# Optimization experiments

Measured on AMD Instinct MI355X. Metric: run time of the kernel, lower is better.

The kernel has to match this reference:

```python
import jax, jax.numpy as jnp
import numpy as np

G, N, E, I, H, O = 128, 1024, 64, 128, 128, 128
EPS = 1e-5


def setup_inputs() -> dict:
    key = jax.random.key(0)
    ks = jax.random.split(key, 6)
    return {
        "feature": jax.random.normal(ks[0], (G, N, I), dtype=jnp.float32),
        "eigen": jax.random.normal(ks[1], (G, N, E), dtype=jnp.float32),
        "weights1": jax.random.normal(ks[2], (E, I, H), dtype=jnp.float32),
        "biases1": jnp.zeros((E, H), dtype=jnp.float32),
        "weights2": jax.random.normal(ks[3], (E, H, O), dtype=jnp.float32),
        "biases2": jnp.zeros((E, O), dtype=jnp.float32),
        "bn_gamma": jnp.ones((O,), dtype=jnp.float32),
        "bn_beta": jnp.zeros((O,), dtype=jnp.float32),
    }


def reference(feature, eigen, weights1, biases1, weights2, biases2, bn_gamma, bn_beta):
    # Eigen projection per graph: [G,E,I]
    spec_in = jnp.einsum('gni,gne->gei', feature, eigen)
    # Per-eigen MLP (grouped small GEMMs)
    spec_hidden = jax.nn.relu(jnp.einsum('eik,gei->gek', weights1, spec_in) + biases1)
    spec_out = jnp.einsum('eko,gek->geo', weights2, spec_hidden) + biases2
    # Inverse projection back to nodes: [G,N,O]
    h = jnp.einsum('geo,gne->gno', spec_out, eigen)
    h = h.reshape(G * N, O)
    # BatchNorm1d in training mode (biased variance over all nodes)
    mean = jnp.mean(h, axis=0)
    var = jnp.mean((h - mean) ** 2, axis=0)
    h = bn_gamma * (h - mean) * jax.lax.rsqrt(var + EPS) + bn_beta
    # Activation + residual (in_dim == out_dim)
    h = jax.nn.relu(h)
    h = feature.reshape(G * N, I) + h
    return h
```

## Files before the change

### kernel.cpp

```cpp
#include <hip/hip_runtime.h>

#define G_ 128
#define N_ 1024
#define E_ 64
#define I_ 128
#define H_ 128
#define O_ 128
#define EPSV 1e-5f

#define WS_SPECIN  0
#define WS_GRAM    4194304
#define WS_ROWSUM  6291456
#define WS_SPECOUT 6324224
#define WS_STATS   7372800
#define WS_SCALE   7373056

__global__ __launch_bounds__(256) void k1_project(
    const float* __restrict__ feature, const float* __restrict__ eigen,
    float* __restrict__ ws)
{
  __shared__ float eig_lds[64][64];
  __shared__ float feat_lds[64][128];
  __shared__ float rs_lds[1024];
  const int g = blockIdx.x;
  const int s = blockIdx.y;
  const int t = threadIdx.x;
  const int h = t >> 7;
  const int u = t & 127;
  const int tr = u >> 4;
  const int tc = u & 15;

  const float4* esrc = (const float4*)(eigen + ((size_t)g * N_ + s * 256) * E_);
  const float4* fsrc = (const float4*)(feature + ((size_t)g * N_ + s * 256) * I_);
  float4* edst = (float4*)(&eig_lds[0][0]);
  float4* fdst = (float4*)(&feat_lds[0][0]);

  float acc[8][8];
  float gr[8][4];
  float rs4[4] = {0.f, 0.f, 0.f, 0.f};
#pragma unroll
  for (int a = 0; a < 8; ++a) {
#pragma unroll
    for (int b = 0; b < 8; ++b) acc[a][b] = 0.f;
#pragma unroll
    for (int b = 0; b < 4; ++b) gr[a][b] = 0.f;
  }

  for (int tile = 0; tile < 4; ++tile) {
    __syncthreads();
#pragma unroll
    for (int j = 0; j < 4; ++j) edst[j * 256 + t] = esrc[tile * 1024 + j * 256 + t];
#pragma unroll
    for (int j = 0; j < 8; ++j) fdst[j * 256 + t] = fsrc[tile * 2048 + j * 256 + t];
    __syncthreads();

    for (int n0 = 0; n0 < 32; ++n0) {
      const int n = h * 32 + n0;
      float4 ea = *(const float4*)&eig_lds[n][8 * tr];
      float4 eb = *(const float4*)&eig_lds[n][8 * tr + 4];
      float4 e2 = *(const float4*)&eig_lds[n][4 * tc];
      float4 fa = *(const float4*)&feat_lds[n][4 * tc];
      float4 fb = *(const float4*)&feat_lds[n][64 + 4 * tc];
      float ev[8] = {ea.x, ea.y, ea.z, ea.w, eb.x, eb.y, eb.z, eb.w};
      float fv[8] = {fa.x, fa.y, fa.z, fa.w, fb.x, fb.y, fb.z, fb.w};
      float e2v[4] = {e2.x, e2.y, e2.z, e2.w};
      rs4[0] += e2v[0]; rs4[1] += e2v[1]; rs4[2] += e2v[2]; rs4[3] += e2v[3];
#pragma unroll
      for (int a = 0; a < 8; ++a) {
#pragma unroll
        for (int b = 0; b < 8; ++b) acc[a][b] = fmaf(ev[a], fv[b], acc[a][b]);
#pragma unroll
        for (int b = 0; b < 4; ++b) gr[a][b] = fmaf(ev[a], e2v[b], gr[a][b]);
      }
    }
  }

  __syncthreads();
  *(float4*)&rs_lds[(h * 8 + tr) * 64 + 4 * tc] =
      make_float4(rs4[0], rs4[1], rs4[2], rs4[3]);
  float* pf = &feat_lds[0][0];
  float* pg = &eig_lds[0][0];
  if (h == 1) {
#pragma unroll
    for (int a = 0; a < 8; ++a) {
      *(float4*)&pf[(a * 2 + 0) * 512 + u * 4] =
          make_float4(acc[a][0], acc[a][1], acc[a][2], acc[a][3]);
      *(float4*)&pf[(a * 2 + 1) * 512 + u * 4] =
          make_float4(acc[a][4], acc[a][5], acc[a][6], acc[a][7]);
      *(float4*)&pg[a * 512 + u * 4] =
          make_float4(gr[a][0], gr[a][1], gr[a][2], gr[a][3]);
    }
  }
  __syncthreads();
  if (h == 0) {
#pragma unroll
    for (int a = 0; a < 8; ++a) {
      float4 p0 = *(const float4*)&pf[(a * 2 + 0) * 512 + u * 4];
      float4 p1 = *(const float4*)&pf[(a * 2 + 1) * 512 + u * 4];
      float4 pgv = *(const float4*)&pg[a * 512 + u * 4];
      acc[a][0] += p0.x; acc[a][1] += p0.y; acc[a][2] += p0.z; acc[a][3] += p0.w;
      acc[a][4] += p1.x; acc[a][5] += p1.y; acc[a][6] += p1.z; acc[a][7] += p1.w;
      gr[a][0] += pgv.x; gr[a][1] += pgv.y; gr[a][2] += pgv.z; gr[a][3] += pgv.w;
      const int e = 8 * tr + a;
      size_t sb = WS_SPECIN + ((size_t)(s * E_ + e) * G_ + g) * I_;
      *(float4*)&ws[sb + 4 * tc] =
          make_float4(acc[a][0], acc[a][1], acc[a][2], acc[a][3]);
      *(float4*)&ws[sb + 64 + 4 * tc] =
          make_float4(acc[a][4], acc[a][5], acc[a][6], acc[a][7]);
      size_t gb = WS_GRAM + ((size_t)(s * G_ + g) * E_ + e) * E_ + 4 * tc;
      *(float4*)&ws[gb] = make_float4(gr[a][0], gr[a][1], gr[a][2], gr[a][3]);
    }
  }
  if (t < 64) {
    ws[WS_ROWSUM + (size_t)(s * G_ + g) * E_ + t] = rs_lds[t] + rs_lds[512 + t];
  }
}

__global__ __launch_bounds__(256) void k2_mlp(
    const float* __restrict__ w1, const float* __restrict__ b1,
    const float* __restrict__ w2, const float* __restrict__ b2,
    float* __restrict__ ws)
{
  __shared__ float Wl[128 * 128];
  __shared__ float XT[128][32];
  __shared__ float HT[128][32];
  const int e = blockIdx.x;
  const int g0 = blockIdx.y * 32;
  const int t = threadIdx.x;
  const int tg = t >> 5;
  const int tk = t & 31;

  {
    const float4* wsrc = (const float4*)(w1 + (size_t)e * I_ * H_);
    float4* wdst = (float4*)Wl;
#pragma unroll
    for (int j = 0; j < 16; ++j) wdst[j * 256 + t] = wsrc[j * 256 + t];
  }
#pragma unroll
  for (int j = 0; j < 4; ++j) {
    int c = j * 256 + t;
    int gl = c >> 5;
    int i4 = (c & 31) * 4;
    size_t base = WS_SPECIN + ((size_t)e * G_ + g0 + gl) * I_ + i4;
    float4 v0 = *(const float4*)&ws[base];
    float4 v1 = *(const float4*)&ws[base + 1048576];
    float4 v2 = *(const float4*)&ws[base + 2097152];
    float4 v3 = *(const float4*)&ws[base + 3145728];
    XT[i4 + 0][gl] = v0.x + v1.x + v2.x + v3.x;
    XT[i4 + 1][gl] = v0.y + v1.y + v2.y + v3.y;
    XT[i4 + 2][gl] = v0.z + v1.z + v2.z + v3.z;
    XT[i4 + 3][gl] = v0.w + v1.w + v2.w + v3.w;
  }
  __syncthreads();

  {
    float4 bb = *(const float4*)&b1[e * H_ + 4 * tk];
    float h[4][4];
#pragma unroll
    for (int a = 0; a < 4; ++a) { h[a][0]=bb.x; h[a][1]=bb.y; h[a][2]=bb.z; h[a][3]=bb.w; }
    for (int i = 0; i < 128; ++i) {
      float4 xv = *(const float4*)&XT[i][4 * tg];
      float4 wr = *(const float4*)&Wl[i * 128 + 4 * tk];
      float xa[4] = {xv.x, xv.y, xv.z, xv.w};
      float wv[4] = {wr.x, wr.y, wr.z, wr.w};
#pragma unroll
      for (int a = 0; a < 4; ++a)
#pragma unroll
        for (int b = 0; b < 4; ++b) h[a][b] = fmaf(xa[a], wv[b], h[a][b]);
    }
#pragma unroll
    for (int a = 0; a < 4; ++a)
#pragma unroll
      for (int b = 0; b < 4; ++b)
        HT[4 * tk + b][4 * tg + a] = fmaxf(h[a][b], 0.f);
  }
  __syncthreads();
  {
    const float4* wsrc = (const float4*)(w2 + (size_t)e * H_ * O_);
    float4* wdst = (float4*)Wl;
#pragma unroll
    for (int j = 0; j < 16; ++j) wdst[j * 256 + t] = wsrc[j * 256 + t];
  }
  __syncthreads();
  {
    float4 bb = *(const float4*)&b2[e * O_ + 4 * tk];
    float o[4][4];
#pragma unroll
    for (int a = 0; a < 4; ++a) { o[a][0]=bb.x; o[a][1]=bb.y; o[a][2]=bb.z; o[a][3]=bb.w; }
    for (int k = 0; k < 128; ++k) {
      float4 hv = *(const float4*)&HT[k][4 * tg];
      float4 wr = *(const float4*)&Wl[k * 128 + 4 * tk];
      float ha[4] = {hv.x, hv.y, hv.z, hv.w};
      float wv[4] = {wr.x, wr.y, wr.z, wr.w};
#pragma unroll
      for (int a = 0; a < 4; ++a)
#pragma unroll
        for (int b = 0; b < 4; ++b) o[a][b] = fmaf(ha[a], wv[b], o[a][b]);
    }
#pragma unroll
    for (int a = 0; a < 4; ++a) {
      size_t ob = WS_SPECOUT + ((size_t)(g0 + 4 * tg + a) * E_ + e) * O_ + 4 * tk;
      *(float4*)&ws[ob] = make_float4(o[a][0], o[a][1], o[a][2], o[a][3]);
    }
  }
}

__global__ __launch_bounds__(256) void k2b_stats(float* __restrict__ ws)
{
  __shared__ float So[64][64];
  __shared__ float Gm[64][64];
  __shared__ float Rsh[64];
  __shared__ float RedM[16][64];
  __shared__ float RedS[16][64];
  const int g = blockIdx.x;
  const int oc = blockIdx.y;
  const int t = threadIdx.x;
  const int tr = t >> 4;
  const int tc = t & 15;

#pragma unroll
  for (int j = 0; j < 4; ++j) {
    int c = j * 256 + t;
    int e = c >> 4;
    int o4 = (c & 15) * 4;
    *(float4*)&So[e][o4] = *(const float4*)&ws[WS_SPECOUT + (size_t)g * E_ * O_ +
                                               (size_t)e * O_ + oc * 64 + o4];
  }
#pragma unroll
  for (int j = 0; j < 4; ++j) {
    int c = j * 256 + t;
    size_t base = WS_GRAM + (size_t)g * 4096 + (size_t)c * 4;
    float4 v0 = *(const float4*)&ws[base];
    float4 v1 = *(const float4*)&ws[base + 524288];
    float4 v2 = *(const float4*)&ws[base + 1048576];
    float4 v3 = *(const float4*)&ws[base + 1572864];
    float4 r;
    r.x = v0.x + v1.x + v2.x + v3.x;
    r.y = v0.y + v1.y + v2.y + v3.y;
    r.z = v0.z + v1.z + v2.z + v3.z;
    r.w = v0.w + v1.w + v2.w + v3.w;
    ((float4*)(&Gm[0][0]))[c] = r;
  }
  if (t < 64) {
    Rsh[t] = ws[WS_ROWSUM + (size_t)g * E_ + t]
           + ws[WS_ROWSUM + 8192 + (size_t)g * E_ + t]
           + ws[WS_ROWSUM + 16384 + (size_t)g * E_ + t]
           + ws[WS_ROWSUM + 24576 + (size_t)g * E_ + t];
  }
  __syncthreads();

  float y[4][4];
#pragma unroll
  for (int a = 0; a < 4; ++a)
#pragma unroll
    for (int b = 0; b < 4; ++b) y[a][b] = 0.f;

  for (int e2 = 0; e2 < 64; ++e2) {
    float4 gv = *(const float4*)&Gm[e2][4 * tr];
    float4 sv = *(const float4*)&So[e2][4 * tc];
    float ga[4] = {gv.x, gv.y, gv.z, gv.w};
    float sb[4] = {sv.x, sv.y, sv.z, sv.w};
#pragma unroll
    for (int a = 0; a < 4; ++a)
#pragma unroll
      for (int b = 0; b < 4; ++b) y[a][b] = fmaf(ga[a], sb[b], y[a][b]);
  }

  float sp[4] = {0.f, 0.f, 0.f, 0.f};
  float sm[4] = {0.f, 0.f, 0.f, 0.f};
#pragma unroll
  for (int a = 0; a < 4; ++a) {
    const int e1 = 4 * tr + a;
    float4 sv = *(const float4*)&So[e1][4 * tc];
    float r = Rsh[e1];
    float sb[4] = {sv.x, sv.y, sv.z, sv.w};
#pragma unroll
    for (int b = 0; b < 4; ++b) {
      sp[b] = fmaf(sb[b], y[a][b], sp[b]);
      sm[b] = fmaf(sb[b], r, sm[b]);
    }
  }
  *(float4*)&RedS[tr][4 * tc] = make_float4(sp[0], sp[1], sp[2], sp[3]);
  *(float4*)&RedM[tr][4 * tc] = make_float4(sm[0], sm[1], sm[2], sm[3]);
  __syncthreads();
  if (t < 64) {
    float ssq = 0.f, smm = 0.f;
#pragma unroll
    for (int w = 0; w < 16; ++w) { ssq += RedS[w][t]; smm += RedM[w][t]; }
    atomicAdd(&ws[WS_STATS + oc * 64 + t], smm);
    atomicAdd(&ws[WS_STATS + 128 + oc * 64 + t], ssq);
  }
}

__global__ void k2c_finalize(const float* __restrict__ gamma, const float* __restrict__ beta,
                             float* __restrict__ ws)
{
  const int t = threadIdx.x;
  if (t < 128) {
    const float inv = 1.f / (float)(G_ * N_);
    float mean = ws[WS_STATS + t] * inv;
    float var = fmaxf(ws[WS_STATS + 128 + t] * inv - mean * mean, 0.f);
    float sc = gamma[t] * rsqrtf(var + EPSV);
    ws[WS_SCALE + t] = sc;
    ws[WS_SCALE + 128 + t] = beta[t] - mean * sc;
  }
}

__global__ __launch_bounds__(256) void k3_output(
    const float* __restrict__ feature, const float* __restrict__ eigen,
    const float* __restrict__ ws, float* __restrict__ out)
{
  __shared__ float Al[64][68];
  __shared__ float Bl[64][128];
  const int g = blockIdx.x;
  const int nb = blockIdx.y * 64;
  const int t = threadIdx.x;
  const int tr = t >> 4;
  const int tc = t & 15;

  {
    const float4* asrc = (const float4*)(eigen + ((size_t)g * N_ + nb) * E_);
#pragma unroll
    for (int j = 0; j < 4; ++j) {
      int c = j * 256 + t;
      *(float4*)&Al[c >> 4][(c & 15) * 4] = asrc[c];
    }
    const float4* bsrc = (const float4*)(ws + WS_SPECOUT + (size_t)g * E_ * O_);
    float4* bdst = (float4*)(&Bl[0][0]);
#pragma unroll
    for (int j = 0; j < 8; ++j) bdst[j * 256 + t] = bsrc[j * 256 + t];
  }
  __syncthreads();

  float acc[4][8];
#pragma unroll
  for (int a = 0; a < 4; ++a)
#pragma unroll
    for (int b = 0; b < 8; ++b) acc[a][b] = 0.f;

  for (int kq = 0; kq < 16; ++kq) {
    const int k0 = 4 * kq;
    float4 a0 = *(const float4*)&Al[tr][k0];
    float4 a1 = *(const float4*)&Al[16 + tr][k0];
    float4 a2 = *(const float4*)&Al[32 + tr][k0];
    float4 a3 = *(const float4*)&Al[48 + tr][k0];
    float am[4][4] = {{a0.x, a0.y, a0.z, a0.w},
                      {a1.x, a1.y, a1.z, a1.w},
                      {a2.x, a2.y, a2.z, a2.w},
                      {a3.x, a3.y, a3.z, a3.w}};
#pragma unroll
    for (int kk = 0; kk < 4; ++kk) {
      float4 bx = *(const float4*)&Bl[k0 + kk][4 * tc];
      float4 by = *(const float4*)&Bl[k0 + kk][64 + 4 * tc];
#pragma unroll
      for (int r = 0; r < 4; ++r) {
        float av = am[r][kk];
        acc[r][0] = fmaf(av, bx.x, acc[r][0]);
        acc[r][1] = fmaf(av, bx.y, acc[r][1]);
        acc[r][2] = fmaf(av, bx.z, acc[r][2]);
        acc[r][3] = fmaf(av, bx.w, acc[r][3]);
        acc[r][4] = fmaf(av, by.x, acc[r][4]);
        acc[r][5] = fmaf(av, by.y, acc[r][5]);
        acc[r][6] = fmaf(av, by.z, acc[r][6]);
        acc[r][7] = fmaf(av, by.w, acc[r][7]);
      }
    }
  }

  float4 sca = *(const float4*)&ws[WS_SCALE + 4 * tc];
  float4 scb = *(const float4*)&ws[WS_SCALE + 64 + 4 * tc];
  float4 sha = *(const float4*)&ws[WS_SCALE + 128 + 4 * tc];
  float4 shb = *(const float4*)&ws[WS_SCALE + 128 + 64 + 4 * tc];
#pragma unroll
  for (int r = 0; r < 4; ++r) {
    const size_t row = (size_t)g * N_ + nb + 16 * r + tr;
    const float* fp = feature + row * I_;
    float* op = out + row * O_;
    float4 f1 = *(const float4*)&fp[4 * tc];
    float4 f2 = *(const float4*)&fp[64 + 4 * tc];
    float4 o1, o2;
    o1.x = f1.x + fmaxf(fmaf(acc[r][0], sca.x, sha.x), 0.f);
    o1.y = f1.y + fmaxf(fmaf(acc[r][1], sca.y, sha.y), 0.f);
    o1.z = f1.z + fmaxf(fmaf(acc[r][2], sca.z, sha.z), 0.f);
    o1.w = f1.w + fmaxf(fmaf(acc[r][3], sca.w, sha.w), 0.f);
    o2.x = f2.x + fmaxf(fmaf(acc[r][4], scb.x, shb.x), 0.f);
    o2.y = f2.y + fmaxf(fmaf(acc[r][5], scb.y, shb.y), 0.f);
    o2.z = f2.z + fmaxf(fmaf(acc[r][6], scb.z, shb.z), 0.f);
    o2.w = f2.w + fmaxf(fmaf(acc[r][7], scb.w, shb.w), 0.f);
    *(float4*)&op[4 * tc] = o1;
    *(float4*)&op[64 + 4 * tc] = o2;
  }
}

extern "C" void kernel_launch(void* const* d_in, const int* in_sizes, int n_in,
                              void* d_out, int out_size, void* d_ws, size_t ws_size,
                              hipStream_t stream) {
  (void)in_sizes; (void)n_in; (void)out_size; (void)ws_size;
  const float* feature = (const float*)d_in[0];
  const float* eigen   = (const float*)d_in[1];
  const float* w1      = (const float*)d_in[2];
  const float* b1      = (const float*)d_in[3];
  const float* w2      = (const float*)d_in[4];
  const float* b2      = (const float*)d_in[5];
  const float* gamma   = (const float*)d_in[6];
  const float* beta    = (const float*)d_in[7];
  float* out = (float*)d_out;
  float* ws  = (float*)d_ws;

  hipMemsetAsync(ws + WS_STATS, 0, 256 * sizeof(float), stream);
  k1_project<<<dim3(G_, 4), 256, 0, stream>>>(feature, eigen, ws);
  k2_mlp<<<dim3(E_, 4), 256, 0, stream>>>(w1, b1, w2, b2, ws);
  k2b_stats<<<dim3(G_, 2), 256, 0, stream>>>(ws);
  k2c_finalize<<<1, 128, 0, stream>>>(gamma, beta, ws);
  k3_output<<<dim3(G_, N_ / 64), 256, 0, stream>>>(feature, eigen, ws, out);
}
```

Baseline: 243.2 us.

## Rewrite eigen projection kernel to use split-bf16 MFMA with swizzled transposed LDS

The projection kernel (feature^T·eigen plus the eigen Gram matrix) moves from scalar FP32 FMAs to 16x16x32 bf16 MFMA instructions. Each FP32 input is split into hi/lo bf16 parts and three MFMAs are issued per tile to keep near-FP32 accuracy. Inputs are stored transposed in LDS with an XOR swizzle to avoid bank conflicts. This trades more instructions and conversion work in the load phase for much higher matrix throughput, but uses strided scalar global loads instead of float4 loads and scalar output stores.

Result: faster. 229.1 us (-5.8%).

```diff
diff --git a/kernel.cpp b/kernel.cpp
--- a/kernel.cpp
+++ b/kernel.cpp
@@ -15,104 +15,142 @@
 #define WS_STATS   7372800
 #define WS_SCALE   7373056
 
+typedef __attribute__((ext_vector_type(4))) float f32x4;
+typedef __attribute__((ext_vector_type(8))) short bf16x8;
+#define MFMA16(a, b, c) __builtin_amdgcn_mfma_f32_16x16x32_bf16((a), (b), (c), 0, 0, 0)
+
+__device__ __forceinline__ unsigned bf16_rne(float x) {
+  unsigned u = __float_as_uint(x);
+  return (u + 0x7fffu + ((u >> 16) & 1u)) >> 16;
+}
+__device__ __forceinline__ void split2(float a, float b, unsigned& hi, unsigned& lo) {
+  unsigned ha = bf16_rne(a), hb = bf16_rne(b);
+  float ra = a - __uint_as_float(ha << 16);
+  float rb = b - __uint_as_float(hb << 16);
+  hi = ha | (hb << 16);
+  lo = bf16_rne(ra) | (bf16_rne(rb) << 16);
+}
+
 __global__ __launch_bounds__(256) void k1_project(
     const float* __restrict__ feature, const float* __restrict__ eigen,
     float* __restrict__ ws)
 {
-  __shared__ float eig_lds[64][64];
-  __shared__ float feat_lds[64][128];
-  __shared__ float rs_lds[1024];
+  __shared__ short ET[2][64][72];
+  __shared__ short FT[2][128][72];
+  __shared__ float rs_lds[4][64];
+
   const int g = blockIdx.x;
   const int s = blockIdx.y;
   const int t = threadIdx.x;
-  const int h = t >> 7;
-  const int u = t & 127;
-  const int tr = u >> 4;
-  const int tc = u & 15;
-
-  const float4* esrc = (const float4*)(eigen + ((size_t)g * N_ + s * 256) * E_);
-  const float4* fsrc = (const float4*)(feature + ((size_t)g * N_ + s * 256) * I_);
-  float4* edst = (float4*)(&eig_lds[0][0]);
-  float4* fdst = (float4*)(&feat_lds[0][0]);
-
-  float acc[8][8];
-  float gr[8][4];
-  float rs4[4] = {0.f, 0.f, 0.f, 0.f};
-#pragma unroll
-  for (int a = 0; a < 8; ++a) {
-#pragma unroll
-    for (int b = 0; b < 8; ++b) acc[a][b] = 0.f;
-#pragma unroll
-    for (int b = 0; b < 4; ++b) gr[a][b] = 0.f;
-  }
-
-  for (int tile = 0; tile < 4; ++tile) {
+  const int l = t & 63;
+  const int w = t >> 6;
+  const int lm = l & 15;
+  const int lk = l >> 4;
+  const size_t nglob = (size_t)g * N_ + (size_t)s * 256;
+
+  const int se = t & 63;
+  const int sng = t >> 6;
+  const int si = t & 127;
+  const int smg = t >> 7;
+
+  f32x4 acc[4][3];
+#pragma unroll
+  for (int m = 0; m < 4; ++m)
+#pragma unroll
+    for (int c = 0; c < 3; ++c) acc[m][c] = (f32x4){0.f, 0.f, 0.f, 0.f};
+
+  float rs = 0.f;
+
+  for (int ch = 0; ch < 4; ++ch) {
     __syncthreads();
-#pragma unroll
-    for (int j = 0; j < 4; ++j) edst[j * 256 + t] = esrc[tile * 1024 + j * 256 + t];
-#pragma unroll
-    for (int j = 0; j < 8; ++j) fdst[j * 256 + t] = fsrc[tile * 2048 + j * 256 + t];
+    const int nb = ch * 64;
+
+    const float* eg = eigen + (nglob + nb) * E_ + se;
+#pragma unroll
+    for (int p = 0; p < 4; ++p) {
+      const int nl = p * 16 + sng * 4;
+      float x0 = eg[(size_t)(nl + 0) * E_];
+      float x1 = eg[(size_t)(nl + 1) * E_];
+      float x2 = eg[(size_t)(nl + 2) * E_];
+      float x3 = eg[(size_t)(nl + 3) * E_];
+      rs += x0 + x1 + x2 + x3;
+      unsigned h01, l01, h23, l23;
+      split2(x0, x1, h01, l01);
+      split2(x2, x3, h23, l23);
+      const int cb = (((nl >> 3) ^ (se >> 3)) << 3) | (nl & 7);
+      *(uint2*)&ET[0][se][cb] = make_uint2(h01, h23);
+      *(uint2*)&ET[1][se][cb] = make_uint2(l01, l23);
+    }
+    const float* fg = feature + (nglob + nb) * I_ + si;
+#pragma unroll
+    for (int p = 0; p < 8; ++p) {
+      const int nl = p * 8 + smg * 4;
+      float x0 = fg[(size_t)(nl + 0) * I_];
+      float x1 = fg[(size_t)(nl + 1) * I_];
+      float x2 = fg[(size_t)(nl + 2) * I_];
+      float x3 = fg[(size_t)(nl + 3) * I_];
+      unsigned h01, l01, h23, l23;
+      split2(x0, x1, h01, l01);
+      split2(x2, x3, h23, l23);
+      const int cb = (((nl >> 3) ^ ((si >> 3) & 7)) << 3) | (nl & 7);
+      *(uint2*)&FT[0][si][cb] = make_uint2(h01, h23);
+      *(uint2*)&FT[1][si][cb] = make_uint2(l01, l23);
+    }
     __syncthreads();
 
-    for (int n0 = 0; n0 < 32; ++n0) {
-      const int n = h * 32 + n0;
-      float4 ea = *(const float4*)&eig_lds[n][8 * tr];
-      float4 eb = *(const float4*)&eig_lds[n][8 * tr + 4];
-      float4 e2 = *(const float4*)&eig_lds[n][4 * tc];
-      float4 fa = *(const float4*)&feat_lds[n][4 * tc];
-      float4 fb = *(const float4*)&feat_lds[n][64 + 4 * tc];
-      float ev[8] = {ea.x, ea.y, ea.z, ea.w, eb.x, eb.y, eb.z, eb.w};
-      float fv[8] = {fa.x, fa.y, fa.z, fa.w, fb.x, fb.y, fb.z, fb.w};
-      float e2v[4] = {e2.x, e2.y, e2.z, e2.w};
-      rs4[0] += e2v[0]; rs4[1] += e2v[1]; rs4[2] += e2v[2]; rs4[3] += e2v[3];
-#pragma unroll
-      for (int a = 0; a < 8; ++a) {
-#pragma unroll
-        for (int b = 0; b < 8; ++b) acc[a][b] = fmaf(ev[a], fv[b], acc[a][b]);
-#pragma unroll
-        for (int b = 0; b < 4; ++b) gr[a][b] = fmaf(ev[a], e2v[b], gr[a][b]);
+#pragma unroll
+    for (int kt = 0; kt < 2; ++kt) {
+      bf16x8 ah[4], al[4];
+#pragma unroll
+      for (int m = 0; m < 4; ++m) {
+        const int er = m * 16 + lm;
+        const int cc = (((kt * 4 + lk) ^ (er >> 3)) << 3);
+        ah[m] = *(const bf16x8*)&ET[0][er][cc];
+        al[m] = *(const bf16x8*)&ET[1][er][cc];
       }
-    }
-  }
-
-  __syncthreads();
-  *(float4*)&rs_lds[(h * 8 + tr) * 64 + 4 * tc] =
-      make_float4(rs4[0], rs4[1], rs4[2], rs4[3]);
-  float* pf = &feat_lds[0][0];
-  float* pg = &eig_lds[0][0];
-  if (h == 1) {
-#pragma unroll
-    for (int a = 0; a < 8; ++a) {
-      *(float4*)&pf[(a * 2 + 0) * 512 + u * 4] =
-          make_float4(acc[a][0], acc[a][1], acc[a][2], acc[a][3]);
-      *(float4*)&pf[(a * 2 + 1) * 512 + u * 4] =
-          make_float4(acc[a][4], acc[a][5], acc[a][6], acc[a][7]);
-      *(float4*)&pg[a * 512 + u * 4] =
-          make_float4(gr[a][0], gr[a][1], gr[a][2], gr[a][3]);
-    }
-  }
-  __syncthreads();
-  if (h == 0) {
-#pragma unroll
-    for (int a = 0; a < 8; ++a) {
-      float4 p0 = *(const float4*)&pf[(a * 2 + 0) * 512 + u * 4];
-      float4 p1 = *(const float4*)&pf[(a * 2 + 1) * 512 + u * 4];
-      float4 pgv = *(const float4*)&pg[a * 512 + u * 4];
-      acc[a][0] += p0.x; acc[a][1] += p0.y; acc[a][2] += p0.z; acc[a][3] += p0.w;
-      acc[a][4] += p1.x; acc[a][5] += p1.y; acc[a][6] += p1.z; acc[a][7] += p1.w;
-      gr[a][0] += pgv.x; gr[a][1] += pgv.y; gr[a][2] += pgv.z; gr[a][3] += pgv.w;
-      const int e = 8 * tr + a;
-      size_t sb = WS_SPECIN + ((size_t)(s * E_ + e) * G_ + g) * I_;
-      *(float4*)&ws[sb + 4 * tc] =
-          make_float4(acc[a][0], acc[a][1], acc[a][2], acc[a][3]);
-      *(float4*)&ws[sb + 64 + 4 * tc] =
-          make_float4(acc[a][4], acc[a][5], acc[a][6], acc[a][7]);
-      size_t gb = WS_GRAM + ((size_t)(s * G_ + g) * E_ + e) * E_ + 4 * tc;
-      *(float4*)&ws[gb] = make_float4(gr[a][0], gr[a][1], gr[a][2], gr[a][3]);
-    }
-  }
+#pragma unroll
+      for (int cl = 0; cl < 3; ++cl) {
+        const int ct = w + cl * 4;
+        const short(*Bh)[72] = (ct < 8) ? FT[0] : ET[0];
+        const short(*Bl)[72] = (ct < 8) ? FT[1] : ET[1];
+        const int br = ((ct < 8) ? ct : (ct - 8)) * 16 + lm;
+        const int cc = (((kt * 4 + lk) ^ ((br >> 3) & 7)) << 3);
+        bf16x8 bh = *(const bf16x8*)&Bh[br][cc];
+        bf16x8 bl = *(const bf16x8*)&Bl[br][cc];
+#pragma unroll
+        for (int m = 0; m < 4; ++m) {
+          acc[m][cl] = MFMA16(ah[m], bh, acc[m][cl]);
+          acc[m][cl] = MFMA16(ah[m], bl, acc[m][cl]);
+          acc[m][cl] = MFMA16(al[m], bh, acc[m][cl]);
+        }
+      }
+    }
+  }
+
+#pragma unroll
+  for (int cl = 0; cl < 3; ++cl) {
+    const int ct = w + cl * 4;
+#pragma unroll
+    for (int m = 0; m < 4; ++m) {
+#pragma unroll
+      for (int r = 0; r < 4; ++r) {
+        const int e = m * 16 + lk * 4 + r;
+        const float v = acc[m][cl][r];
+        if (ct < 8) {
+          const int i = ct * 16 + lm;
+          ws[WS_SPECIN + ((size_t)(s * E_ + e) * G_ + g) * I_ + i] = v;
+        } else {
+          const int e2 = (ct - 8) * 16 + lm;
+          ws[WS_GRAM + ((size_t)(s * G_ + g) * E_ + e) * E_ + e2] = v;
+        }
+      }
+    }
+  }
+  rs_lds[sng][se] = rs;
+  __syncthreads();
   if (t < 64) {
-    ws[WS_ROWSUM + (size_t)(s * G_ + g) * E_ + t] = rs_lds[t] + rs_lds[512 + t];
+    ws[WS_ROWSUM + (size_t)(s * G_ + g) * E_ + t] =
+        rs_lds[0][t] + rs_lds[1][t] + rs_lds[2][t] + rs_lds[3][t];
   }
 }
 
@@ -286,7 +324,7 @@
   if (t < 64) {
     float ssq = 0.f, smm = 0.f;
 #pragma unroll
-    for (int w = 0; w < 16; ++w) { ssq += RedS[w][t]; smm += RedM[w][t]; }
+    for (int wv = 0; wv < 16; ++wv) { ssq += RedS[wv][t]; smm += RedM[wv][t]; }
     atomicAdd(&ws[WS_STATS + oc * 64 + t], smm);
     atomicAdd(&ws[WS_STATS + 128 + oc * 64 + t], ssq);
   }
```
